# Optimization experiments

Measured on AMD Instinct MI355X. Metric: run time of the kernel, lower is better.

The kernel has to match this reference:

```python
import jax, jax.numpy as jnp
import numpy as np
import math

B, S, D = 1, 4096, 1024
H, DK = 16, 64
WINDOW = 256
GLOBAL = 16


def setup_inputs() -> dict:
    key = jax.random.key(0)
    ks = jax.random.split(key, 8)
    scale = 1.0 / math.sqrt(D)  # xavier-ish scale for projections
    return {
        "query": jax.random.normal(ks[0], (B, S, D), jnp.float32),
        "key": jax.random.normal(ks[1], (B, S, D), jnp.float32),
        "value": jax.random.normal(ks[2], (B, S, D), jnp.float32),
        "Wq": jax.random.normal(ks[3], (D, D), jnp.float32) * scale,
        "bq": jnp.zeros((D,), jnp.float32),
        "Wk": jax.random.normal(ks[4], (D, D), jnp.float32) * scale,
        "bk": jnp.zeros((D,), jnp.float32),
        "Wv": jax.random.normal(ks[5], (D, D), jnp.float32) * scale,
        "bv": jnp.zeros((D,), jnp.float32),
        "Wo": jax.random.normal(ks[6], (D, D), jnp.float32) * scale,
        "bo": jnp.zeros((D,), jnp.float32),
    }


def _split_heads(x):
    # [B, S, D] -> [B, H, S, DK]
    return x.reshape(B, S, H, DK).transpose(0, 2, 1, 3)


def reference(query, key, value, Wq, bq, Wk, bk, Wv, bv, Wo, bo):
    Q = _split_heads(query @ Wq + bq)   # [B,H,S,DK]
    K = _split_heads(key @ Wk + bk)
    V = _split_heads(value @ Wv + bv)

    scores = jnp.einsum("bhqd,bhkd->bhqk", Q, K) / math.sqrt(DK)  # [B,H,S,S]

    i = jnp.arange(S)[:, None]
    j = jnp.arange(S)[None, :]
    local = jnp.abs(i - j) <= WINDOW
    glob = (i < GLOBAL) | (j < GLOBAL)
    causal = j <= i
    mask = (local | glob) & causal  # [S,S]

    scores = jnp.where(mask[None, None], scores, -jnp.inf)
    probs = jax.nn.softmax(scores, axis=-1)  # dropout is identity (p=0 / eval)

    out = jnp.einsum("bhqk,bhkd->bhqd", probs, V)  # [B,H,S,DK]
    out = out.transpose(0, 2, 1, 3).reshape(B, S, D)
    return out @ Wo + bo
```

## Files before the change

### kernel.cpp

```cpp
#include <hip/hip_runtime.h>

typedef __bf16 bf16_t;
typedef __attribute__((ext_vector_type(8))) __bf16 bf16x8;
typedef __attribute__((ext_vector_type(4))) __bf16 bf16x4;
typedef __attribute__((ext_vector_type(2))) __bf16 bf16x2;
typedef __attribute__((ext_vector_type(4))) float f32x4;

#define S_LEN 4096
#define D_MODEL 1024
#define NH 16
#define DKH 64
#define WIN 256
#define NGLOB 16
#define HSZ (S_LEN * DKH)

__device__ inline void g2l16(const void* g, void* l) {
  __builtin_amdgcn_global_load_lds(
      (__attribute__((address_space(1))) void*)(void*)g,
      (__attribute__((address_space(3))) void*)l, 16, 0, 0);
}

template <int DUMMY>
__device__ __forceinline__ void gemm_body(const bf16_t* __restrict__ A,
                                          const bf16_t* __restrict__ Bt,
                                          int m0, int n0, int wave, int lane,
                                          bf16_t* As, bf16_t* Bs,
                                          f32x4 acc[2][4]) {
  const int wr = wave >> 1, wc = wave & 1;
#pragma unroll
  for (int i = 0; i < 2; i++)
#pragma unroll
    for (int j = 0; j < 4; j++) acc[i][j] = {0.f, 0.f, 0.f, 0.f};
  const int ssl = (lane & 7) ^ (lane >> 3);
  const int srow = 2 * (lane >> 3) + (ssl >> 2);
  const int scol = 8 * (ssl & 3);
  const int fr = lane & 15;
  const int fkg = lane >> 4;

  for (int k0 = 0; k0 < D_MODEL; k0 += 32) {
    {
      const int row0 = wave * 16;
      g2l16(A + (size_t)(m0 + row0 + srow) * D_MODEL + k0 + scol,
            &As[wave * 512]);
    }
#pragma unroll
    for (int i = 0; i < 2; i++) {
      const int c = wave * 2 + i;
      g2l16(Bt + (size_t)(n0 + c * 16 + srow) * D_MODEL + k0 + scol,
            &Bs[c * 512]);
    }
    __syncthreads();
    bf16x8 af[2], bfr[4];
#pragma unroll
    for (int m = 0; m < 2; m++) {
      const int rr = wr * 32 + m * 16 + fr;
      af[m] = *(const bf16x8*)&As[(rr >> 1) * 64 +
                                  ((((rr & 1) << 2) + fkg) ^ ((rr >> 1) & 7)) *
                                      8];
    }
#pragma unroll
    for (int n = 0; n < 4; n++) {
      const int rr = wc * 64 + n * 16 + fr;
      bfr[n] = *(const bf16x8*)&Bs[(rr >> 1) * 64 +
                                   ((((rr & 1) << 2) + fkg) ^ ((rr >> 1) & 7)) *
                                       8];
    }
#pragma unroll
    for (int m = 0; m < 2; m++)
#pragma unroll
      for (int n = 0; n < 4; n++)
        acc[m][n] = __builtin_amdgcn_mfma_f32_16x16x32_bf16(af[m], bfr[n],
                                                            acc[m][n], 0, 0, 0);
    __syncthreads();
  }
}

__global__ __launch_bounds__(256) void gemm_qkv(
    const bf16_t* __restrict__ Xq, const bf16_t* __restrict__ Xk,
    const bf16_t* __restrict__ Xv, const bf16_t* __restrict__ Wt,
    const float* __restrict__ bq, const float* __restrict__ bk,
    const float* __restrict__ bv, bf16_t* __restrict__ Qo,
    bf16_t* __restrict__ Ko, bf16_t* __restrict__ Vto) {
  __shared__ bf16_t As[64 * 32];
  __shared__ bf16_t Bs[128 * 32];
  const int lin = blockIdx.x;
  const int wg = ((lin & 7) * 192) + (lin >> 3);
  const int n0 = (wg & 7) * 128;
  const int m0 = ((wg >> 3) & 63) * 64;
  const int which = wg >> 9;

  const bf16_t* A = which == 0 ? Xq : which == 1 ? Xk : Xv;
  const bf16_t* Bt = Wt + (size_t)which * (D_MODEL * D_MODEL);
  const float* bias = which == 0 ? bq : which == 1 ? bk : bv;

  const int wave = threadIdx.x >> 6, lane = threadIdx.x & 63;
  f32x4 acc[2][4];
  gemm_body<0>(A, Bt, m0, n0, wave, lane, As, Bs, acc);

  const int wr = wave >> 1, wc = wave & 1;
  const int cr = (lane >> 4) * 4;
  const int cc = lane & 15;
#pragma unroll
  for (int m = 0; m < 2; m++) {
    const int rowg = m0 + wr * 32 + m * 16 + cr;
#pragma unroll
    for (int n = 0; n < 4; n++) {
      const int colg = n0 + wc * 64 + n * 16 + cc;
      const float bv_ = bias[colg];
      const int h = colg >> 6, d = colg & 63;
#pragma unroll
      for (int r = 0; r < 4; r++) {
        const int s = rowg + r;
        const float v = acc[m][n][r] + bv_;
        if (which == 0)
          Qo[h * HSZ + s * DKH + d] = (bf16_t)(v * 0.125f);
        else if (which == 1)
          Ko[h * HSZ + s * DKH + d] = (bf16_t)v;
        else
          Vto[h * HSZ + d * S_LEN + s] = (bf16_t)v;
      }
    }
  }
}

__global__ __launch_bounds__(256) void gemm_out(const bf16_t* __restrict__ A_,
                                                const bf16_t* __restrict__ Bt_,
                                                const float* __restrict__ bias,
                                                float* __restrict__ Cout) {
  __shared__ bf16_t As[64 * 32];
  __shared__ bf16_t Bs[128 * 32];
  const int lin = blockIdx.x;
  const int wg = ((lin & 7) * 64) + (lin >> 3);
  const int n0 = (wg & 7) * 128;
  const int m0 = (wg >> 3) * 64;
  const int wave = threadIdx.x >> 6, lane = threadIdx.x & 63;
  f32x4 acc[2][4];
  gemm_body<0>(A_, Bt_, m0, n0, wave, lane, As, Bs, acc);

  const int wr = wave >> 1, wc = wave & 1;
  const int cr = (lane >> 4) * 4;
  const int cc = lane & 15;
#pragma unroll
  for (int m = 0; m < 2; m++) {
    const int rowg = m0 + wr * 32 + m * 16 + cr;
#pragma unroll
    for (int n = 0; n < 4; n++) {
      const int colg = n0 + wc * 64 + n * 16 + cc;
      const float bv_ = bias[colg];
#pragma unroll
      for (int r = 0; r < 4; r++)
        Cout[(size_t)(rowg + r) * D_MODEL + colg] = acc[m][n][r] + bv_;
    }
  }
}

__global__ void convx3(const float* __restrict__ q, const float* __restrict__ k,
                       const float* __restrict__ v, bf16_t* __restrict__ oq,
                       bf16_t* __restrict__ ok, bf16_t* __restrict__ ov) {
  const float* in = blockIdx.y == 0 ? q : blockIdx.y == 1 ? k : v;
  bf16_t* out = blockIdx.y == 0 ? oq : blockIdx.y == 1 ? ok : ov;
  const int i = (blockIdx.x * 256 + threadIdx.x) * 4;
  const float4 x = *(const float4*)&in[i];
  bf16x4 o = {(bf16_t)x.x, (bf16_t)x.y, (bf16_t)x.z, (bf16_t)x.w};
  *(bf16x4*)&out[i] = o;
}

__global__ void convw(const float* __restrict__ W0, const float* __restrict__ W1,
                      const float* __restrict__ W2, const float* __restrict__ W3,
                      bf16_t* __restrict__ out) {
  __shared__ float t[64][65];
  const float* W = blockIdx.z == 0 ? W0 : blockIdx.z == 1 ? W1
                  : blockIdx.z == 2 ? W2 : W3;
  bf16_t* Wt = out + (size_t)blockIdx.z * (D_MODEL * D_MODEL);
  const int k0 = blockIdx.y * 64, n0 = blockIdx.x * 64;
  const int tx = threadIdx.x & 63, ty = threadIdx.x >> 6;
#pragma unroll
  for (int i = 0; i < 16; i++) {
    const int r = i * 4 + ty;
    t[r][tx] = W[(size_t)(k0 + r) * D_MODEL + n0 + tx];
  }
  __syncthreads();
#pragma unroll
  for (int i = 0; i < 16; i++) {
    const int r = i * 4 + ty;
    Wt[(size_t)(n0 + r) * D_MODEL + k0 + tx] = (bf16_t)t[tx][r];
  }
}

__global__ __launch_bounds__(256) void attn_kern(const bf16_t* __restrict__ Q,
                                                 const bf16_t* __restrict__ K,
                                                 const bf16_t* __restrict__ V,
                                                 bf16_t* __restrict__ O) {
  __shared__ bf16_t p_lds[4][16 * 40];
  const int wave = threadIdx.x >> 6, lane = threadIdx.x & 63;
  const int h = blockIdx.y;
  const int q0 = blockIdx.x * 64 + wave * 16;
  const bf16_t* Qh = Q + h * HSZ;
  const bf16_t* Kh = K + h * HSZ;
  const bf16_t* Vh = V + h * HSZ;

  const int fr = lane & 15;
  const int fk = (lane >> 4) * 8;
  const int cr = (lane >> 4) * 4;

  const bf16x8 aq0 = *(const bf16x8*)&Qh[(q0 + fr) * DKH + fk];
  const bf16x8 aq1 = *(const bf16x8*)&Qh[(q0 + fr) * DKH + 32 + fk];

  f32x4 acc_o[4];
#pragma unroll
  for (int i = 0; i < 4; i++) acc_o[i] = {0.f, 0.f, 0.f, 0.f};
  float m_run = -1e30f, l_run = 0.f;

  const int kt_end = (q0 + 15) >> 5;
  int kt_lo = (q0 - WIN) >> 5;
  if (kt_lo < 0) kt_lo = 0;
  const int nt = kt_end - kt_lo + 1 + (kt_lo > 0 ? 1 : 0);

#define TILE_KB(t) ((kt_lo > 0) ? ((t) == 0 ? 0 : (kt_lo + (t)-1) * 32) : (t)*32)
#define LOADK(kb, A0, A1, A2, A3)                              \
  A0 = *(const bf16x8*)&Kh[((kb) + fr) * DKH + fk];            \
  A1 = *(const bf16x8*)&Kh[((kb) + fr) * DKH + 32 + fk];       \
  A2 = *(const bf16x8*)&Kh[((kb) + 16 + fr) * DKH + fk];       \
  A3 = *(const bf16x8*)&Kh[((kb) + 16 + fr) * DKH + 32 + fk];

  bf16x8 kc0, kc1, kc2, kc3;
  {
    const int kb0 = TILE_KB(0);
    LOADK(kb0, kc0, kc1, kc2, kc3)
  }

  const int iq = q0 + fr;
  bf16_t* prow = &p_lds[wave][fr * 40];
  const bf16x8* pread = (const bf16x8*)&p_lds[wave][fr * 40 + fk];

  for (int t = 0; t < nt; t++) {
    const int kb = TILE_KB(t);
    bf16x8 kn0, kn1, kn2, kn3;
    const bool have_next = (t + 1 < nt);
    if (have_next) {
      const int nkb = TILE_KB(t + 1);
      LOADK(nkb, kn0, kn1, kn2, kn3)
    }
    bf16x8 vf0 = *(const bf16x8*)&Vh[(0 * 16 + fr) * S_LEN + kb + fk];
    bf16x8 vf1 = *(const bf16x8*)&Vh[(1 * 16 + fr) * S_LEN + kb + fk];
    bf16x8 vf2 = *(const bf16x8*)&Vh[(2 * 16 + fr) * S_LEN + kb + fk];
    bf16x8 vf3 = *(const bf16x8*)&Vh[(3 * 16 + fr) * S_LEN + kb + fk];

    f32x4 s0 = {0.f, 0.f, 0.f, 0.f}, s1 = {0.f, 0.f, 0.f, 0.f};
    s0 = __builtin_amdgcn_mfma_f32_16x16x32_bf16(kc0, aq0, s0, 0, 0, 0);
    s0 = __builtin_amdgcn_mfma_f32_16x16x32_bf16(kc1, aq1, s0, 0, 0, 0);
    s1 = __builtin_amdgcn_mfma_f32_16x16x32_bf16(kc2, aq0, s1, 0, 0, 0);
    s1 = __builtin_amdgcn_mfma_f32_16x16x32_bf16(kc3, aq1, s1, 0, 0, 0);

    float v[8];
#pragma unroll
    for (int r = 0; r < 4; r++) {
      const int j0 = kb + cr + r, j1 = j0 + 16;
      v[r] = (j0 <= iq && (iq - j0 <= WIN || j0 < NGLOB)) ? s0[r] : -1e30f;
      v[4 + r] = (j1 <= iq && (iq - j1 <= WIN || j1 < NGLOB)) ? s1[r] : -1e30f;
    }
    float mt = fmaxf(fmaxf(fmaxf(v[0], v[1]), fmaxf(v[2], v[3])),
                     fmaxf(fmaxf(v[4], v[5]), fmaxf(v[6], v[7])));
    mt = fmaxf(mt, __shfl_xor(mt, 16));
    mt = fmaxf(mt, __shfl_xor(mt, 32));
    const float mn = fmaxf(m_run, mt);
    const float alpha = __expf(m_run - mn);
    m_run = mn;
    float p[8];
    float ps = 0.f;
#pragma unroll
    for (int i = 0; i < 8; i++) {
      p[i] = __expf(v[i] - mn);
      ps += p[i];
    }
    ps += __shfl_xor(ps, 16);
    ps += __shfl_xor(ps, 32);
    l_run = l_run * alpha + ps;

    *(bf16x2*)&prow[cr] = bf16x2{(bf16_t)p[0], (bf16_t)p[1]};
    *(bf16x2*)&prow[cr + 2] = bf16x2{(bf16_t)p[2], (bf16_t)p[3]};
    *(bf16x2*)&prow[16 + cr] = bf16x2{(bf16_t)p[4], (bf16_t)p[5]};
    *(bf16x2*)&prow[16 + cr + 2] = bf16x2{(bf16_t)p[6], (bf16_t)p[7]};

    float alpha_r[4];
#pragma unroll
    for (int r = 0; r < 4; r++) alpha_r[r] = __shfl(alpha, cr + r);

    asm volatile("" ::: "memory");
    const bf16x8 pa = *pread;
    asm volatile("" ::: "memory");

#pragma unroll
    for (int fd = 0; fd < 4; fd++) {
#pragma unroll
      for (int r = 0; r < 4; r++) acc_o[fd][r] *= alpha_r[r];
    }
    acc_o[0] = __builtin_amdgcn_mfma_f32_16x16x32_bf16(pa, vf0, acc_o[0], 0, 0, 0);
    acc_o[1] = __builtin_amdgcn_mfma_f32_16x16x32_bf16(pa, vf1, acc_o[1], 0, 0, 0);
    acc_o[2] = __builtin_amdgcn_mfma_f32_16x16x32_bf16(pa, vf2, acc_o[2], 0, 0, 0);
    acc_o[3] = __builtin_amdgcn_mfma_f32_16x16x32_bf16(pa, vf3, acc_o[3], 0, 0, 0);

    if (have_next) {
      kc0 = kn0; kc1 = kn1; kc2 = kn2; kc3 = kn3;
    }
  }

  const float linv = 1.0f / l_run;
  float inv_r[4];
#pragma unroll
  for (int r = 0; r < 4; r++) inv_r[r] = __shfl(linv, cr + r);

#pragma unroll
  for (int fd = 0; fd < 4; fd++)
#pragma unroll
    for (int r = 0; r < 4; r++) {
      const int s = q0 + cr + r;
      O[(size_t)s * D_MODEL + h * DKH + fd * 16 + fr] =
          (bf16_t)(acc_o[fd][r] * inv_r[r]);
    }
}

extern "C" void kernel_launch(void* const* d_in, const int* in_sizes, int n_in,
                              void* d_out, int out_size, void* d_ws,
                              size_t ws_size, hipStream_t stream) {
  const float* query = (const float*)d_in[0];
  const float* key = (const float*)d_in[1];
  const float* value = (const float*)d_in[2];
  const float* Wq = (const float*)d_in[3];
  const float* bq = (const float*)d_in[4];
  const float* Wk = (const float*)d_in[5];
  const float* bk = (const float*)d_in[6];
  const float* Wv = (const float*)d_in[7];
  const float* bv = (const float*)d_in[8];
  const float* Wo = (const float*)d_in[9];
  const float* bo = (const float*)d_in[10];

  char* ws = (char*)d_ws;
  bf16_t* Qb = (bf16_t*)(ws);
  bf16_t* Kb = (bf16_t*)(ws + (8ull << 20));
  bf16_t* Vtb = (bf16_t*)(ws + (16ull << 20));
  bf16_t* Wt = (bf16_t*)(ws + (24ull << 20));
  bf16_t* Xq = (bf16_t*)(ws + (32ull << 20));
  bf16_t* Xk = (bf16_t*)(ws + (40ull << 20));
  bf16_t* Xv = (bf16_t*)(ws + (48ull << 20));
  bf16_t* Ab = (bf16_t*)(ws + (56ull << 20));

  const size_t WSTRIDE = (size_t)D_MODEL * D_MODEL;

  convw<<<dim3(16, 16, 4), 256, 0, stream>>>(Wq, Wk, Wv, Wo, Wt);
  convx3<<<dim3(4096, 3), 256, 0, stream>>>(query, key, value, Xq, Xk, Xv);

  gemm_qkv<<<1536, 256, 0, stream>>>(Xq, Xk, Xv, Wt, bq, bk, bv, Qb, Kb, Vtb);

  attn_kern<<<dim3(64, 16), 256, 0, stream>>>(Qb, Kb, Vtb, Ab);

  gemm_out<<<512, 256, 0, stream>>>(Ab, Wt + 3 * WSTRIDE, bo, (float*)d_out);
}
```

Baseline: 139.6 us.

## Fuse fp32 input conversion into QKV GEMM with double-buffered 128x128 tiles

Drops the separate convx3 kernel: the QKV GEMM now reads fp32 activations directly, converts them to bf16 in registers and writes them to LDS. Both GEMMs move from 64x128 to 128x128 tiles with double-buffered LDS, prefetching the next K-slice while MFMAs run on the current one, and use launch bounds of 3 blocks. This removes a full read/write pass over the activations and improves reuse and latency hiding, at the cost of more registers and LDS per block and half as many blocks.

```diff
diff --git a/kernel.cpp b/kernel.cpp
--- a/kernel.cpp
+++ b/kernel.cpp
@@ -20,89 +20,147 @@
       (__attribute__((address_space(3))) void*)l, 16, 0, 0);
 }
 
-template <int DUMMY>
-__device__ __forceinline__ void gemm_body(const bf16_t* __restrict__ A,
+template <bool AF32>
+__device__ __forceinline__ void gemm_pipe(const void* __restrict__ Ap,
                                           const bf16_t* __restrict__ Bt,
                                           int m0, int n0, int wave, int lane,
                                           bf16_t* As, bf16_t* Bs,
-                                          f32x4 acc[2][4]) {
+                                          f32x4 acc[4][4]) {
+  const float* Af = (const float*)Ap;
+  const bf16_t* Ah = (const bf16_t*)Ap;
   const int wr = wave >> 1, wc = wave & 1;
 #pragma unroll
-  for (int i = 0; i < 2; i++)
+  for (int i = 0; i < 4; i++)
 #pragma unroll
     for (int j = 0; j < 4; j++) acc[i][j] = {0.f, 0.f, 0.f, 0.f};
+
+  const int arow_l = lane >> 2;
+  const int aslot = lane & 3;
   const int ssl = (lane & 7) ^ (lane >> 3);
-  const int srow = 2 * (lane >> 3) + (ssl >> 2);
-  const int scol = 8 * (ssl & 3);
+  const int srowB = 2 * (lane >> 3) + (ssl >> 2);
+  const int scolB = 8 * (ssl & 3);
   const int fr = lane & 15;
   const int fkg = lane >> 4;
 
-  for (int k0 = 0; k0 < D_MODEL; k0 += 32) {
-    {
-      const int row0 = wave * 16;
-      g2l16(A + (size_t)(m0 + row0 + srow) * D_MODEL + k0 + scol,
-            &As[wave * 512]);
-    }
-#pragma unroll
-    for (int i = 0; i < 2; i++) {
-      const int c = wave * 2 + i;
-      g2l16(Bt + (size_t)(n0 + c * 16 + srow) * D_MODEL + k0 + scol,
-            &Bs[c * 512]);
-    }
-    __syncthreads();
-    bf16x8 af[2], bfr[4];
-#pragma unroll
-    for (int m = 0; m < 2; m++) {
-      const int rr = wr * 32 + m * 16 + fr;
-      af[m] = *(const bf16x8*)&As[(rr >> 1) * 64 +
-                                  ((((rr & 1) << 2) + fkg) ^ ((rr >> 1) & 7)) *
-                                      8];
+#define A_LDS_OFF(c)                                                       \
+  ((((c)*16 + arow_l) >> 1) * 64 +                                         \
+   (((((c)*16 + arow_l) & 1) << 2 | aslot) ^ ((((c)*16 + arow_l) >> 1) & 7)) * 8)
+
+#pragma unroll
+  for (int i = 0; i < 2; i++) {
+    const int c = wave * 2 + i;
+    const int r = c * 16 + arow_l;
+    if constexpr (AF32) {
+      const float* s = Af + (size_t)(m0 + r) * D_MODEL + aslot * 8;
+      const float4 x = *(const float4*)s;
+      const float4 y = *(const float4*)(s + 4);
+      bf16x8 w = {(bf16_t)x.x, (bf16_t)x.y, (bf16_t)x.z, (bf16_t)x.w,
+                  (bf16_t)y.x, (bf16_t)y.y, (bf16_t)y.z, (bf16_t)y.w};
+      *(bf16x8*)&As[A_LDS_OFF(c)] = w;
+    } else {
+      *(bf16x8*)&As[A_LDS_OFF(c)] =
+          *(const bf16x8*)(Ah + (size_t)(m0 + r) * D_MODEL + aslot * 8);
+    }
+    g2l16(Bt + (size_t)(n0 + c * 16 + srowB) * D_MODEL + scolB, &Bs[c * 512]);
+  }
+  __syncthreads();
+
+#pragma unroll 2
+  for (int t = 0; t < 32; ++t) {
+    const int buf = t & 1;
+    const bool hn = (t < 31);
+    float4 ax0{}, ay0{}, ax1{}, ay1{};
+    bf16x8 ah0{}, ah1{};
+    if (hn) {
+      const int kn = (t + 1) * 32;
+      {
+        const int r0 = (wave * 2) * 16 + arow_l;
+        const int r1 = (wave * 2 + 1) * 16 + arow_l;
+        if constexpr (AF32) {
+          const float* s0 = Af + (size_t)(m0 + r0) * D_MODEL + kn + aslot * 8;
+          const float* s1 = Af + (size_t)(m0 + r1) * D_MODEL + kn + aslot * 8;
+          ax0 = *(const float4*)s0;
+          ay0 = *(const float4*)(s0 + 4);
+          ax1 = *(const float4*)s1;
+          ay1 = *(const float4*)(s1 + 4);
+        } else {
+          ah0 = *(const bf16x8*)(Ah + (size_t)(m0 + r0) * D_MODEL + kn + aslot * 8);
+          ah1 = *(const bf16x8*)(Ah + (size_t)(m0 + r1) * D_MODEL + kn + aslot * 8);
+        }
+        g2l16(Bt + (size_t)(n0 + (wave * 2) * 16 + srowB) * D_MODEL + kn + scolB,
+              &Bs[(buf ^ 1) * 4096 + (wave * 2) * 512]);
+        g2l16(Bt + (size_t)(n0 + (wave * 2 + 1) * 16 + srowB) * D_MODEL + kn + scolB,
+              &Bs[(buf ^ 1) * 4096 + (wave * 2 + 1) * 512]);
+      }
+    }
+    __builtin_amdgcn_sched_barrier(0);
+    bf16x8 af[4], bfr[4];
+#pragma unroll
+    for (int m = 0; m < 4; m++) {
+      const int rr = wr * 64 + m * 16 + fr;
+      af[m] = *(const bf16x8*)&As[buf * 4096 + (rr >> 1) * 64 +
+                                  ((((rr & 1) << 2) + fkg) ^ ((rr >> 1) & 7)) * 8];
     }
 #pragma unroll
     for (int n = 0; n < 4; n++) {
       const int rr = wc * 64 + n * 16 + fr;
-      bfr[n] = *(const bf16x8*)&Bs[(rr >> 1) * 64 +
-                                   ((((rr & 1) << 2) + fkg) ^ ((rr >> 1) & 7)) *
-                                       8];
-    }
-#pragma unroll
-    for (int m = 0; m < 2; m++)
+      bfr[n] = *(const bf16x8*)&Bs[buf * 4096 + (rr >> 1) * 64 +
+                                   ((((rr & 1) << 2) + fkg) ^ ((rr >> 1) & 7)) * 8];
+    }
+#pragma unroll
+    for (int m = 0; m < 4; m++)
 #pragma unroll
       for (int n = 0; n < 4; n++)
         acc[m][n] = __builtin_amdgcn_mfma_f32_16x16x32_bf16(af[m], bfr[n],
                                                             acc[m][n], 0, 0, 0);
+    __builtin_amdgcn_sched_barrier(0);
+    if (hn) {
+      bf16x8 w0, w1;
+      if constexpr (AF32) {
+        w0 = bf16x8{(bf16_t)ax0.x, (bf16_t)ax0.y, (bf16_t)ax0.z, (bf16_t)ax0.w,
+                    (bf16_t)ay0.x, (bf16_t)ay0.y, (bf16_t)ay0.z, (bf16_t)ay0.w};
+        w1 = bf16x8{(bf16_t)ax1.x, (bf16_t)ax1.y, (bf16_t)ax1.z, (bf16_t)ax1.w,
+                    (bf16_t)ay1.x, (bf16_t)ay1.y, (bf16_t)ay1.z, (bf16_t)ay1.w};
+      } else {
+        w0 = ah0;
+        w1 = ah1;
+      }
+      *(bf16x8*)&As[(buf ^ 1) * 4096 + A_LDS_OFF(wave * 2)] = w0;
+      *(bf16x8*)&As[(buf ^ 1) * 4096 + A_LDS_OFF(wave * 2 + 1)] = w1;
+    }
     __syncthreads();
   }
-}
-
-__global__ __launch_bounds__(256) void gemm_qkv(
-    const bf16_t* __restrict__ Xq, const bf16_t* __restrict__ Xk,
-    const bf16_t* __restrict__ Xv, const bf16_t* __restrict__ Wt,
+#undef A_LDS_OFF
+}
+
+__global__ __launch_bounds__(256, 3) void gemm_qkv(
+    const float* __restrict__ Xq, const float* __restrict__ Xk,
+    const float* __restrict__ Xv, const bf16_t* __restrict__ Wt,
     const float* __restrict__ bq, const float* __restrict__ bk,
     const float* __restrict__ bv, bf16_t* __restrict__ Qo,
     bf16_t* __restrict__ Ko, bf16_t* __restrict__ Vto) {
-  __shared__ bf16_t As[64 * 32];
-  __shared__ bf16_t Bs[128 * 32];
+  __shared__ bf16_t As[2 * 128 * 32];
+  __shared__ bf16_t Bs[2 * 128 * 32];
   const int lin = blockIdx.x;
-  const int wg = ((lin & 7) * 192) + (lin >> 3);
+  const int wg = ((lin & 7) * 96) + (lin >> 3);
   const int n0 = (wg & 7) * 128;
-  const int m0 = ((wg >> 3) & 63) * 64;
-  const int which = wg >> 9;
-
-  const bf16_t* A = which == 0 ? Xq : which == 1 ? Xk : Xv;
+  const int m0 = ((wg >> 3) & 31) * 128;
+  const int which = wg >> 8;
+
+  const float* A = which == 0 ? Xq : which == 1 ? Xk : Xv;
   const bf16_t* Bt = Wt + (size_t)which * (D_MODEL * D_MODEL);
   const float* bias = which == 0 ? bq : which == 1 ? bk : bv;
 
   const int wave = threadIdx.x >> 6, lane = threadIdx.x & 63;
-  f32x4 acc[2][4];
-  gemm_body<0>(A, Bt, m0, n0, wave, lane, As, Bs, acc);
+  f32x4 acc[4][4];
+  gemm_pipe<true>(A, Bt, m0, n0, wave, lane, As, Bs, acc);
 
   const int wr = wave >> 1, wc = wave & 1;
   const int cr = (lane >> 4) * 4;
   const int cc = lane & 15;
 #pragma unroll
-  for (int m = 0; m < 2; m++) {
-    const int rowg = m0 + wr * 32 + m * 16 + cr;
+  for (int m = 0; m < 4; m++) {
+    const int rowg = m0 + wr * 64 + m * 16 + cr;
 #pragma unroll
     for (int n = 0; n < 4; n++) {
       const int colg = n0 + wc * 64 + n * 16 + cc;
@@ -123,26 +181,25 @@
   }
 }
 
-__global__ __launch_bounds__(256) void gemm_out(const bf16_t* __restrict__ A_,
-                                                const bf16_t* __restrict__ Bt_,
-                                                const float* __restrict__ bias,
-                                                float* __restrict__ Cout) {
-  __shared__ bf16_t As[64 * 32];
-  __shared__ bf16_t Bs[128 * 32];
+__global__ __launch_bounds__(256, 3) void gemm_out(
+    const bf16_t* __restrict__ A_, const bf16_t* __restrict__ Bt_,
+    const float* __restrict__ bias, float* __restrict__ Cout) {
+  __shared__ bf16_t As[2 * 128 * 32];
+  __shared__ bf16_t Bs[2 * 128 * 32];
   const int lin = blockIdx.x;
-  const int wg = ((lin & 7) * 64) + (lin >> 3);
+  const int wg = ((lin & 7) * 32) + (lin >> 3);
   const int n0 = (wg & 7) * 128;
-  const int m0 = (wg >> 3) * 64;
+  const int m0 = (wg >> 3) * 128;
   const int wave = threadIdx.x >> 6, lane = threadIdx.x & 63;
-  f32x4 acc[2][4];
-  gemm_body<0>(A_, Bt_, m0, n0, wave, lane, As, Bs, acc);
+  f32x4 acc[4][4];
+  gemm_pipe<false>(A_, Bt_, m0, n0, wave, lane, As, Bs, acc);
 
   const int wr = wave >> 1, wc = wave & 1;
   const int cr = (lane >> 4) * 4;
   const int cc = lane & 15;
 #pragma unroll
-  for (int m = 0; m < 2; m++) {
-    const int rowg = m0 + wr * 32 + m * 16 + cr;
+  for (int m = 0; m < 4; m++) {
+    const int rowg = m0 + wr * 64 + m * 16 + cr;
 #pragma unroll
     for (int n = 0; n < 4; n++) {
       const int colg = n0 + wc * 64 + n * 16 + cc;
@@ -152,17 +209,6 @@
         Cout[(size_t)(rowg + r) * D_MODEL + colg] = acc[m][n][r] + bv_;
     }
   }
-}
-
-__global__ void convx3(const float* __restrict__ q, const float* __restrict__ k,
-                       const float* __restrict__ v, bf16_t* __restrict__ oq,
-                       bf16_t* __restrict__ ok, bf16_t* __restrict__ ov) {
-  const float* in = blockIdx.y == 0 ? q : blockIdx.y == 1 ? k : v;
-  bf16_t* out = blockIdx.y == 0 ? oq : blockIdx.y == 1 ? ok : ov;
-  const int i = (blockIdx.x * 256 + threadIdx.x) * 4;
-  const float4 x = *(const float4*)&in[i];
-  bf16x4 o = {(bf16_t)x.x, (bf16_t)x.y, (bf16_t)x.z, (bf16_t)x.w};
-  *(bf16x4*)&out[i] = o;
 }
 
 __global__ void convw(const float* __restrict__ W0, const float* __restrict__ W1,
@@ -340,19 +386,16 @@
   bf16_t* Kb = (bf16_t*)(ws + (8ull << 20));
   bf16_t* Vtb = (bf16_t*)(ws + (16ull << 20));
   bf16_t* Wt = (bf16_t*)(ws + (24ull << 20));
-  bf16_t* Xq = (bf16_t*)(ws + (32ull << 20));
-  bf16_t* Xk = (bf16_t*)(ws + (40ull << 20));
-  bf16_t* Xv = (bf16_t*)(ws + (48ull << 20));
-  bf16_t* Ab = (bf16_t*)(ws + (56ull << 20));
+  bf16_t* Ab = (bf16_t*)(ws + (32ull << 20));
 
   const size_t WSTRIDE = (size_t)D_MODEL * D_MODEL;
 
   convw<<<dim3(16, 16, 4), 256, 0, stream>>>(Wq, Wk, Wv, Wo, Wt);
-  convx3<<<dim3(4096, 3), 256, 0, stream>>>(query, key, value, Xq, Xk, Xv);
-
-  gemm_qkv<<<1536, 256, 0, stream>>>(Xq, Xk, Xv, Wt, bq, bk, bv, Qb, Kb, Vtb);
+
+  gemm_qkv<<<768, 256, 0, stream>>>(query, key, value, Wt, bq, bk, bv, Qb, Kb,
+                                    Vtb);
 
   attn_kern<<<dim3(64, 16), 256, 0, stream>>>(Qb, Kb, Vtb, Ab);
 
-  gemm_out<<<512, 256, 0, stream>>>(Ab, Wt + 3 * WSTRIDE, bo, (float*)d_out);
-}
+  gemm_out<<<256, 256, 0, stream>>>(Ab, Wt + 3 * WSTRIDE, bo, (float*)d_out);
+}
```

Result: faster. 129.1 us (-7.5%).

## Rewrite QKV GEMM with 256x256 double-buffered tiles and enlarge output GEMM tile

Applied to the files above, without the earlier changes.

The QKV projection GEMM becomes a 512-thread kernel computing 256x256 tiles. It stages K=64 slices into double-buffered LDS with explicit vmcnt waits, prefetches the next tiles while computing the current one, and raises MFMA priority with setprio. The output GEMM grows its tile from 64x128 to 128x128. The aim is more data reuse per LDS load and less global-load latency exposure. The cost is far fewer workgroups (192 and 256), which may leave CUs underused, plus heavy register and LDS pressure.

```diff
diff --git a/kernel.cpp b/kernel.cpp
--- a/kernel.cpp
+++ b/kernel.cpp
@@ -20,89 +20,124 @@
       (__attribute__((address_space(3))) void*)l, 16, 0, 0);
 }
 
-template <int DUMMY>
-__device__ __forceinline__ void gemm_body(const bf16_t* __restrict__ A,
-                                          const bf16_t* __restrict__ Bt,
-                                          int m0, int n0, int wave, int lane,
-                                          bf16_t* As, bf16_t* Bs,
-                                          f32x4 acc[2][4]) {
-  const int wr = wave >> 1, wc = wave & 1;
-#pragma unroll
-  for (int i = 0; i < 2; i++)
-#pragma unroll
-    for (int j = 0; j < 4; j++) acc[i][j] = {0.f, 0.f, 0.f, 0.f};
-  const int ssl = (lane & 7) ^ (lane >> 3);
-  const int srow = 2 * (lane >> 3) + (ssl >> 2);
-  const int scol = 8 * (ssl & 3);
-  const int fr = lane & 15;
-  const int fkg = lane >> 4;
-
-  for (int k0 = 0; k0 < D_MODEL; k0 += 32) {
-    {
-      const int row0 = wave * 16;
-      g2l16(A + (size_t)(m0 + row0 + srow) * D_MODEL + k0 + scol,
-            &As[wave * 512]);
-    }
-#pragma unroll
-    for (int i = 0; i < 2; i++) {
-      const int c = wave * 2 + i;
-      g2l16(Bt + (size_t)(n0 + c * 16 + srow) * D_MODEL + k0 + scol,
-            &Bs[c * 512]);
-    }
-    __syncthreads();
-    bf16x8 af[2], bfr[4];
-#pragma unroll
-    for (int m = 0; m < 2; m++) {
-      const int rr = wr * 32 + m * 16 + fr;
-      af[m] = *(const bf16x8*)&As[(rr >> 1) * 64 +
-                                  ((((rr & 1) << 2) + fkg) ^ ((rr >> 1) & 7)) *
-                                      8];
-    }
-#pragma unroll
-    for (int n = 0; n < 4; n++) {
-      const int rr = wc * 64 + n * 16 + fr;
-      bfr[n] = *(const bf16x8*)&Bs[(rr >> 1) * 64 +
-                                   ((((rr & 1) << 2) + fkg) ^ ((rr >> 1) & 7)) *
-                                       8];
-    }
-#pragma unroll
-    for (int m = 0; m < 2; m++)
-#pragma unroll
-      for (int n = 0; n < 4; n++)
-        acc[m][n] = __builtin_amdgcn_mfma_f32_16x16x32_bf16(af[m], bfr[n],
-                                                            acc[m][n], 0, 0, 0);
-    __syncthreads();
-  }
-}
-
-__global__ __launch_bounds__(256) void gemm_qkv(
+__global__ __launch_bounds__(512, 2) void gemm_qkv(
     const bf16_t* __restrict__ Xq, const bf16_t* __restrict__ Xk,
     const bf16_t* __restrict__ Xv, const bf16_t* __restrict__ Wt,
     const float* __restrict__ bq, const float* __restrict__ bk,
     const float* __restrict__ bv, bf16_t* __restrict__ Qo,
     bf16_t* __restrict__ Ko, bf16_t* __restrict__ Vto) {
-  __shared__ bf16_t As[64 * 32];
-  __shared__ bf16_t Bs[128 * 32];
+  __shared__ bf16_t As[2 * 2 * 128 * 64];
+  __shared__ bf16_t Bs[2 * 2 * 128 * 64];
+
   const int lin = blockIdx.x;
-  const int wg = ((lin & 7) * 192) + (lin >> 3);
-  const int n0 = (wg & 7) * 128;
-  const int m0 = ((wg >> 3) & 63) * 64;
-  const int which = wg >> 9;
+  const int wg = ((lin & 7) * 24) + (lin >> 3);
+  const int which = wg >> 6;
+  const int rem = wg & 63;
+  const int n0 = (rem & 3) * 256;
+  const int m0 = (rem >> 2) * 256;
 
   const bf16_t* A = which == 0 ? Xq : which == 1 ? Xk : Xv;
   const bf16_t* Bt = Wt + (size_t)which * (D_MODEL * D_MODEL);
   const float* bias = which == 0 ? bq : which == 1 ? bk : bv;
 
-  const int wave = threadIdx.x >> 6, lane = threadIdx.x & 63;
-  f32x4 acc[2][4];
-  gemm_body<0>(A, Bt, m0, n0, wave, lane, As, Bs, acc);
-
-  const int wr = wave >> 1, wc = wave & 1;
+  const int tid = threadIdx.x;
+  const int wid = tid >> 6, lane = tid & 63;
+  const int wr = wid >> 2, wc = wid & 3;
+  const int fr = lane & 15, fkg = lane >> 4;
+
+  const int idx0 = tid, idx1 = 512 + tid;
+  const int r0 = idx0 >> 3, sc0 = (((idx0 & 7) ^ (r0 & 7)) * 8);
+  const int r1 = idx1 >> 3, sc1 = (((idx1 & 7) ^ (r1 & 7)) * 8);
+
+#define STAGE_A(u, half)                                                      \
+  {                                                                           \
+    g2l16(A + (size_t)(m0 + (half)*128 + r0) * D_MODEL + (u)*64 + sc0,        \
+          &As[((u)&1) * 16384 + (half)*8192 + idx0 * 8]);                     \
+    g2l16(A + (size_t)(m0 + (half)*128 + r1) * D_MODEL + (u)*64 + sc1,        \
+          &As[((u)&1) * 16384 + (half)*8192 + idx1 * 8]);                     \
+  }
+#define STAGE_B(u, half)                                                      \
+  {                                                                           \
+    g2l16(Bt + (size_t)(n0 + (half)*128 + r0) * D_MODEL + (u)*64 + sc0,       \
+          &Bs[((u)&1) * 16384 + (half)*8192 + idx0 * 8]);                     \
+    g2l16(Bt + (size_t)(n0 + (half)*128 + r1) * D_MODEL + (u)*64 + sc1,       \
+          &Bs[((u)&1) * 16384 + (half)*8192 + idx1 * 8]);                     \
+  }
+
+  f32x4 acc[8][4];
+#pragma unroll
+  for (int i = 0; i < 8; i++)
+#pragma unroll
+    for (int j = 0; j < 4; j++) acc[i][j] = {0.f, 0.f, 0.f, 0.f};
+
+  STAGE_A(0, 0) STAGE_A(0, 1) STAGE_B(0, 0) STAGE_B(0, 1)
+  STAGE_A(1, 0) STAGE_A(1, 1)
+
+  const int abase = wr * 8192;
+  const int bbase = (wc >> 1) * 8192;
+
+  for (int u = 0; u < 16; ++u) {
+    const int bufo = (u & 1) * 16384;
+    asm volatile("" ::: "memory");
+    if (u < 15)
+      asm volatile("s_waitcnt vmcnt(4)" ::: "memory");
+    else
+      asm volatile("s_waitcnt vmcnt(0)" ::: "memory");
+    __builtin_amdgcn_s_barrier();
+    asm volatile("" ::: "memory");
+    if (u + 1 < 16) { STAGE_B(u + 1, 0) STAGE_B(u + 1, 1) }
+
+    bf16x8 a0[8], a1[8], b0[4];
+#pragma unroll
+    for (int m = 0; m < 8; m++) {
+      const int rh = m * 16 + fr;
+      a0[m] = *(const bf16x8*)&As[bufo + abase + rh * 64 +
+                                  ((fkg ^ (rh & 7)) * 8)];
+      a1[m] = *(const bf16x8*)&As[bufo + abase + rh * 64 +
+                                  (((4 + fkg) ^ (rh & 7)) * 8)];
+    }
+#pragma unroll
+    for (int n = 0; n < 4; n++) {
+      const int rh = (wc & 1) * 64 + n * 16 + fr;
+      b0[n] = *(const bf16x8*)&Bs[bufo + bbase + rh * 64 +
+                                  ((fkg ^ (rh & 7)) * 8)];
+    }
+    __builtin_amdgcn_s_setprio(1);
+#pragma unroll
+    for (int m = 0; m < 8; m++)
+#pragma unroll
+      for (int n = 0; n < 4; n++)
+        acc[m][n] = __builtin_amdgcn_mfma_f32_16x16x32_bf16(a0[m], b0[n],
+                                                            acc[m][n], 0, 0, 0);
+    __builtin_amdgcn_s_setprio(0);
+
+    asm volatile("s_waitcnt lgkmcnt(0)" ::: "memory");
+    __builtin_amdgcn_s_barrier();
+    asm volatile("" ::: "memory");
+    if (u + 2 < 16) { STAGE_A(u + 2, 0) STAGE_A(u + 2, 1) }
+
+    bf16x8 b1[4];
+#pragma unroll
+    for (int n = 0; n < 4; n++) {
+      const int rh = (wc & 1) * 64 + n * 16 + fr;
+      b1[n] = *(const bf16x8*)&Bs[bufo + bbase + rh * 64 +
+                                  (((4 + fkg) ^ (rh & 7)) * 8)];
+    }
+    __builtin_amdgcn_s_setprio(1);
+#pragma unroll
+    for (int m = 0; m < 8; m++)
+#pragma unroll
+      for (int n = 0; n < 4; n++)
+        acc[m][n] = __builtin_amdgcn_mfma_f32_16x16x32_bf16(a1[m], b1[n],
+                                                            acc[m][n], 0, 0, 0);
+    __builtin_amdgcn_s_setprio(0);
+  }
+
   const int cr = (lane >> 4) * 4;
   const int cc = lane & 15;
 #pragma unroll
-  for (int m = 0; m < 2; m++) {
-    const int rowg = m0 + wr * 32 + m * 16 + cr;
+  for (int m = 0; m < 8; m++) {
+    const int rowg = m0 + wr * 128 + m * 16 + cr;
 #pragma unroll
     for (int n = 0; n < 4; n++) {
       const int colg = n0 + wc * 64 + n * 16 + cc;
@@ -121,28 +156,82 @@
       }
     }
   }
+#undef STAGE_A
+#undef STAGE_B
+}
+
+__device__ __forceinline__ void gemm_body(const bf16_t* __restrict__ Ah,
+                                          const bf16_t* __restrict__ Bt,
+                                          int m0, int n0, int wave, int lane,
+                                          bf16_t* As, bf16_t* Bs,
+                                          f32x4 acc[4][4]) {
+  const int wr = wave >> 1, wc = wave & 1;
+#pragma unroll
+  for (int i = 0; i < 4; i++)
+#pragma unroll
+    for (int j = 0; j < 4; j++) acc[i][j] = {0.f, 0.f, 0.f, 0.f};
+
+  const int ssl = (lane & 7) ^ (lane >> 3);
+  const int srowB = 2 * (lane >> 3) + (ssl >> 2);
+  const int scolB = 8 * (ssl & 3);
+  const int fr = lane & 15;
+  const int fkg = lane >> 4;
+
+  for (int k0 = 0; k0 < D_MODEL; k0 += 32) {
+#pragma unroll
+    for (int i = 0; i < 2; i++) {
+      const int c = wave * 2 + i;
+      g2l16(Bt + (size_t)(n0 + c * 16 + srowB) * D_MODEL + k0 + scolB,
+            &Bs[c * 512]);
+      g2l16(Ah + (size_t)(m0 + c * 16 + srowB) * D_MODEL + k0 + scolB,
+            &As[c * 512]);
+    }
+    __syncthreads();
+    bf16x8 af[4], bfr[4];
+#pragma unroll
+    for (int m = 0; m < 4; m++) {
+      const int rr = wr * 64 + m * 16 + fr;
+      af[m] = *(const bf16x8*)&As[(rr >> 1) * 64 +
+                                  ((((rr & 1) << 2) + fkg) ^ ((rr >> 1) & 7)) *
+                                      8];
+    }
+#pragma unroll
+    for (int n = 0; n < 4; n++) {
+      const int rr = wc * 64 + n * 16 + fr;
+      bfr[n] = *(const bf16x8*)&Bs[(rr >> 1) * 64 +
+                                   ((((rr & 1) << 2) + fkg) ^ ((rr >> 1) & 7)) *
+                                       8];
+    }
+#pragma unroll
+    for (int m = 0; m < 4; m++)
+#pragma unroll
+      for (int n = 0; n < 4; n++)
+        acc[m][n] = __builtin_amdgcn_mfma_f32_16x16x32_bf16(af[m], bfr[n],
+                                                            acc[m][n], 0, 0, 0);
+    __syncthreads();
+  }
 }
 
 __global__ __launch_bounds__(256) void gemm_out(const bf16_t* __restrict__ A_,
                                                 const bf16_t* __restrict__ Bt_,
                                                 const float* __restrict__ bias,
                                                 float* __restrict__ Cout) {
-  __shared__ bf16_t As[64 * 32];
+  __shared__ bf16_t As[128 * 32];
   __shared__ bf16_t Bs[128 * 32];
   const int lin = blockIdx.x;
-  const int wg = ((lin & 7) * 64) + (lin >> 3);
+  const int wg = ((lin & 7) * 32) + (lin >> 3);
   const int n0 = (wg & 7) * 128;
-  const int m0 = (wg >> 3) * 64;
+  const int m0 = (wg >> 3) * 128;
   const int wave = threadIdx.x >> 6, lane = threadIdx.x & 63;
-  f32x4 acc[2][4];
-  gemm_body<0>(A_, Bt_, m0, n0, wave, lane, As, Bs, acc);
+  f32x4 acc[4][4];
+  gemm_body(A_, Bt_, m0, n0, wave, lane, As, Bs, acc);
 
   const int wr = wave >> 1, wc = wave & 1;
   const int cr = (lane >> 4) * 4;
   const int cc = lane & 15;
 #pragma unroll
-  for (int m = 0; m < 2; m++) {
-    const int rowg = m0 + wr * 32 + m * 16 + cr;
+  for (int m = 0; m < 4; m++) {
+    const int rowg = m0 + wr * 64 + m * 16 + cr;
 #pragma unroll
     for (int n = 0; n < 4; n++) {
       const int colg = n0 + wc * 64 + n * 16 + cc;
@@ -350,9 +439,9 @@
   convw<<<dim3(16, 16, 4), 256, 0, stream>>>(Wq, Wk, Wv, Wo, Wt);
   convx3<<<dim3(4096, 3), 256, 0, stream>>>(query, key, value, Xq, Xk, Xv);
 
-  gemm_qkv<<<1536, 256, 0, stream>>>(Xq, Xk, Xv, Wt, bq, bk, bv, Qb, Kb, Vtb);
+  gemm_qkv<<<192, 512, 0, stream>>>(Xq, Xk, Xv, Wt, bq, bk, bv, Qb, Kb, Vtb);
 
   attn_kern<<<dim3(64, 16), 256, 0, stream>>>(Qb, Kb, Vtb, Ab);
 
-  gemm_out<<<512, 256, 0, stream>>>(Ab, Wt + 3 * WSTRIDE, bo, (float*)d_out);
-}
+  gemm_out<<<256, 256, 0, stream>>>(Ab, Wt + 3 * WSTRIDE, bo, (float*)d_out);
+}
```

Result: slower. 143.1 us (+2.5%).
